# Optimization experiments

Hardware: AMD Instinct MI355X
Metric: run time of the kernel (lower is better)

The kernel has to match this reference:

```python
import jax, jax.numpy as jnp
import numpy as np

# norse LICell parameters: tau_mem_inv given as 1/0.001; others at norse defaults
DT = 0.001          # LICell default dt (module's self.dt is never passed to the cell)
TAU_MEM_INV = 1000.0
TAU_SYN_INV = 200.0
V_LEAK = 0.0


def setup_inputs() -> dict:
    key = jax.random.key(0)
    k1, k2 = jax.random.split(key)
    x = jax.random.normal(k1, (256, 1, 512, 512), dtype=jnp.float32)   # [T, C=1, H, W]
    kernel = jax.random.normal(k2, (5, 5), dtype=jnp.float32)          # square conv kernel
    return {"x": x, "kernel": kernel}


def reference(x, kernel):
    T, C, H, W = x.shape

    # Leaky-integrator (norse li_feed_forward_step) over time:
    #   v' = v + dt*tau_mem_inv*((v_leak - v) + i)
    #   i' = i - dt*tau_syn_inv*i + x_t
    # output at each step is v'.
    def step(carry, xt):
        v, i = carry
        v_new = v + DT * TAU_MEM_INV * ((V_LEAK - v) + i)
        i_new = i - DT * TAU_SYN_INV * i + xt
        return (v_new, i_new), v_new

    zeros = jnp.zeros((C, H, W), x.dtype)
    _, vs = jax.lax.scan(step, (zeros, zeros), x)  # [T, C, H, W]

    # Per-timestep 1->1 channel conv with 'same' padding, batched over T at once.
    k = kernel.shape[0]
    pad = (k - 1) // 2
    w = kernel[None, None]  # [O=1, I=1, k, k]
    out = jax.lax.conv_general_dilated(
        vs, w, window_strides=(1, 1),
        padding=[(pad, pad), (pad, pad)],
        dimension_numbers=("NCHW", "OIHW", "NCHW"),
    )
    return out  # [T, 1, H, W]
```

## Files before the change

### kernel.cpp

```cpp
#include <hip/hip_runtime.h>

#define T_STEPS 256
#define IMG 512
#define HW (IMG * IMG)
#define TW 32
#define TH 8
#define HTW 40
#define HTH 12
#define NCHK 120
#define BUF_DW 512
#define NBUF 12

__device__ __align__(16) float g_zeropage[8] = {0, 0, 0, 0, 0, 0, 0, 0};

typedef const __attribute__((address_space(1))) unsigned int* gptr_t;
typedef __attribute__((address_space(3))) unsigned int* lptr_t;
typedef float vf4 __attribute__((ext_vector_type(4)));

__launch_bounds__(64)
__global__ void conv_li_kernel(const float* __restrict__ x,
                               const float* __restrict__ kern,
                               float* __restrict__ out) {
    __shared__ __align__(16) float lds[NBUF][BUF_DW];
    const int tid = threadIdx.x;
    const int bid = blockIdx.x;
    const int vbid = (bid & 7) * 128 + (bid >> 3);
    const int bx = vbid & 15;
    const int by = vbid >> 4;

    float kw[25];
#pragma unroll
    for (int i = 0; i < 25; ++i)
        kw[i] = __int_as_float(__builtin_amdgcn_readfirstlane(__float_as_int(kern[i])));

    const float* srcA; const float* srcB; bool okA, okB;
    {
        int c = tid;
        int row = c / 10, cc = c - row * 10;
        int gy = by * TH + row - 2, gx = bx * TW + cc * 4 - 4;
        okA = (gy >= 0) && (gy < IMG) && (gx >= 0) && (gx <= IMG - 4);
        srcA = x + (size_t)(okA ? gy : 0) * IMG + (okA ? gx : 0);
        c = tid + 64;
        row = c / 10; cc = c - row * 10;
        gy = by * TH + row - 2; gx = bx * TW + cc * 4 - 4;
        okB = (c < NCHK) && (gy >= 0) && (gy < IMG) && (gx >= 0) && (gx <= IMG - 4);
        srcB = x + (size_t)(okB ? gy : 0) * IMG + (okB ? gx : 0);
    }

    auto GLDS = [&](int bi, int tf) {
        const float* pA = okA ? srcA + (size_t)tf * HW : g_zeropage;
        const float* pB = okB ? srcB + (size_t)tf * HW : g_zeropage;
        __builtin_amdgcn_global_load_lds((gptr_t)pA, (lptr_t)&lds[bi][0], 16, 0, 0);
        __builtin_amdgcn_global_load_lds((gptr_t)pB, (lptr_t)&lds[bi][256], 16, 0, 0);
    };
    auto BATCH = [&](int bufbase, int f0) {
#pragma unroll
        for (int j = 0; j < 4; ++j) {
            int tf = f0 + j; if (tf > T_STEPS - 1) tf = T_STEPS - 1;
            GLDS(bufbase + j, tf);
        }
    };

    const int q = tid & 7;
    const int rr = tid >> 3;
    const size_t obase = (size_t)(by * TH + rr) * IMG + bx * TW + q * 4;

    vf4 st = {0.f, 0.f, 0.f, 0.f};

    auto STEP = [&](int bi, int t) {
        float ax = 0.f, ay = 0.f, az = 0.f, aw = 0.f;
        const float* Bp = &lds[bi][rr * HTW + q * 4];
#pragma unroll
        for (int dy = 0; dy < 5; ++dy) {
            const float* L = Bp + dy * HTW;
            vf4 d0 = *(const vf4*)(L);
            vf4 d1 = *(const vf4*)(L + 4);
            vf4 d2 = *(const vf4*)(L + 8);
            const float e2 = d0.z, e3 = d0.w, e4 = d1.x, e5 = d1.y;
            const float e6 = d1.z, e7 = d1.w, e8 = d2.x, e9 = d2.y;
            const float k0 = kw[dy * 5 + 0], k1 = kw[dy * 5 + 1], k2 = kw[dy * 5 + 2];
            const float k3 = kw[dy * 5 + 3], k4 = kw[dy * 5 + 4];
            ax = fmaf(k0, e2, ax); ax = fmaf(k1, e3, ax); ax = fmaf(k2, e4, ax);
            ax = fmaf(k3, e5, ax); ax = fmaf(k4, e6, ax);
            ay = fmaf(k0, e3, ay); ay = fmaf(k1, e4, ay); ay = fmaf(k2, e5, ay);
            ay = fmaf(k3, e6, ay); ay = fmaf(k4, e7, ay);
            az = fmaf(k0, e4, az); az = fmaf(k1, e5, az); az = fmaf(k2, e6, az);
            az = fmaf(k3, e7, az); az = fmaf(k4, e8, az);
            aw = fmaf(k0, e5, aw); aw = fmaf(k1, e6, aw); aw = fmaf(k2, e7, aw);
            aw = fmaf(k3, e8, aw); aw = fmaf(k4, e9, aw);
        }
        vf4 s = st;
        __builtin_nontemporal_store(s, (vf4*)(out + (size_t)t * HW + obase));
        st.x = st.x - 0.2f * st.x + ax;
        st.y = st.y - 0.2f * st.y + ay;
        st.z = st.z - 0.2f * st.z + az;
        st.w = st.w - 0.2f * st.w + aw;
    };

    BATCH(0, 0);
    BATCH(4, 4);

    asm volatile("s_waitcnt vmcnt(8)" ::: "memory");
    STEP(0, 0); STEP(1, 1); STEP(2, 2); STEP(3, 3);
    BATCH(8, 8);

#pragma clang loop unroll(disable)
    for (int sg = 0; sg < 21; ++sg) {
        const int t0 = 4 + sg * 12;
        asm volatile("s_waitcnt vmcnt(12)" ::: "memory");
        STEP(4, t0 + 0); STEP(5, t0 + 1); STEP(6, t0 + 2); STEP(7, t0 + 3);
        BATCH(0, t0 + 8);
        asm volatile("s_waitcnt vmcnt(12)" ::: "memory");
        STEP(8, t0 + 4); STEP(9, t0 + 5); STEP(10, t0 + 6); STEP(11, t0 + 7);
        BATCH(4, t0 + 12);
        asm volatile("s_waitcnt vmcnt(12)" ::: "memory");
        STEP(0, t0 + 8); STEP(1, t0 + 9); STEP(2, t0 + 10); STEP(3, t0 + 11);
        BATCH(8, t0 + 16);
    }
}

extern "C" void kernel_launch(void* const* d_in, const int* in_sizes, int n_in,
                              void* d_out, int out_size, void* d_ws, size_t ws_size,
                              hipStream_t stream) {
    const float* x = (const float*)d_in[0];
    const float* kern = (const float*)d_in[1];
    float* out = (float*)d_out;

    conv_li_kernel<<<dim3(1024), dim3(64), 0, stream>>>(x, kern, out);
}
```

Before: 98.90 us.

## Widen conv tile to 64 columns with eight outputs per thread and deeper prefetch

Each block now covers a 64x8 output tile instead of 32x8, so the grid is halved and every thread computes eight adjacent outputs. The halo tile is loaded with four direct-to-LDS loads per lane into 12 frames using a padded row stride of 21 chunks. The pipeline now keeps three four-frame batches in flight instead of two. The aim is less redundant halo traffic and more arithmetic per LDS read. The cost is fewer waves per CU, a larger LDS footprint and more registers per thread, which may leave less room to hide memory latency in this bandwidth-bound kernel.

Result: slower. 160.4 us (+62.2%).

```diff
diff --git a/kernel.cpp b/kernel.cpp
--- a/kernel.cpp
+++ b/kernel.cpp
@@ -3,13 +3,13 @@
 #define T_STEPS 256
 #define IMG 512
 #define HW (IMG * IMG)
-#define TW 32
+#define TW 64
 #define TH 8
-#define HTW 40
+#define ROWCHK 18
+#define ROWSTRIDE 21
 #define HTH 12
-#define NCHK 120
-#define BUF_DW 512
-#define NBUF 12
+#define FRAME_DW 1024
+#define NFRAME 12
 
 __device__ __align__(16) float g_zeropage[8] = {0, 0, 0, 0, 0, 0, 0, 0};
 
@@ -21,101 +21,103 @@
 __global__ void conv_li_kernel(const float* __restrict__ x,
                                const float* __restrict__ kern,
                                float* __restrict__ out) {
-    __shared__ __align__(16) float lds[NBUF][BUF_DW];
+    __shared__ __align__(16) float lds[NFRAME * FRAME_DW];
     const int tid = threadIdx.x;
     const int bid = blockIdx.x;
-    const int vbid = (bid & 7) * 128 + (bid >> 3);
-    const int bx = vbid & 15;
-    const int by = vbid >> 4;
+    const int vbid = (bid & 7) * 64 + (bid >> 3);
+    const int bx = vbid & 7;
+    const int by = vbid >> 3;
 
     float kw[25];
 #pragma unroll
     for (int i = 0; i < 25; ++i)
         kw[i] = __int_as_float(__builtin_amdgcn_readfirstlane(__float_as_int(kern[i])));
 
-    const float* srcA; const float* srcB; bool okA, okB;
-    {
-        int c = tid;
-        int row = c / 10, cc = c - row * 10;
-        int gy = by * TH + row - 2, gx = bx * TW + cc * 4 - 4;
-        okA = (gy >= 0) && (gy < IMG) && (gx >= 0) && (gx <= IMG - 4);
-        srcA = x + (size_t)(okA ? gy : 0) * IMG + (okA ? gx : 0);
-        c = tid + 64;
-        row = c / 10; cc = c - row * 10;
-        gy = by * TH + row - 2; gx = bx * TW + cc * 4 - 4;
-        okB = (c < NCHK) && (gy >= 0) && (gy < IMG) && (gx >= 0) && (gx <= IMG - 4);
-        srcB = x + (size_t)(okB ? gy : 0) * IMG + (okB ? gx : 0);
+    const float* src[4]; bool ok[4];
+#pragma unroll
+    for (int k = 0; k < 4; ++k) {
+        int s = k * 64 + tid;
+        int row = s / ROWSTRIDE, cc = s - row * ROWSTRIDE;
+        int gy = by * TH + row - 2;
+        int gx = bx * TW + cc * 4 - 4;
+        ok[k] = (row < HTH) && (cc < ROWCHK) &&
+                (gy >= 0) && (gy < IMG) && (gx >= 0) && (gx <= IMG - 4);
+        src[k] = x + (size_t)(ok[k] ? gy : 0) * IMG + (ok[k] ? gx : 0);
     }
 
-    auto GLDS = [&](int bi, int tf) {
-        const float* pA = okA ? srcA + (size_t)tf * HW : g_zeropage;
-        const float* pB = okB ? srcB + (size_t)tf * HW : g_zeropage;
-        __builtin_amdgcn_global_load_lds((gptr_t)pA, (lptr_t)&lds[bi][0], 16, 0, 0);
-        __builtin_amdgcn_global_load_lds((gptr_t)pB, (lptr_t)&lds[bi][256], 16, 0, 0);
+    auto GLDS = [&](int fi, int tf) {
+        float* fb = &lds[fi * FRAME_DW];
+#pragma unroll
+        for (int k = 0; k < 4; ++k) {
+            const float* p = ok[k] ? src[k] + (size_t)tf * HW : g_zeropage;
+            __builtin_amdgcn_global_load_lds((gptr_t)p, (lptr_t)(fb + k * 256), 16, 0, 0);
+        }
     };
-    auto BATCH = [&](int bufbase, int f0) {
+    auto BATCH = [&](int fbase, int f0) {
 #pragma unroll
         for (int j = 0; j < 4; ++j) {
             int tf = f0 + j; if (tf > T_STEPS - 1) tf = T_STEPS - 1;
-            GLDS(bufbase + j, tf);
+            GLDS(fbase + j, tf);
         }
     };
 
     const int q = tid & 7;
     const int rr = tid >> 3;
-    const size_t obase = (size_t)(by * TH + rr) * IMG + bx * TW + q * 4;
+    const size_t obase = (size_t)(by * TH + rr) * IMG + bx * TW + q * 8;
 
-    vf4 st = {0.f, 0.f, 0.f, 0.f};
+    float st[8] = {0.f, 0.f, 0.f, 0.f, 0.f, 0.f, 0.f, 0.f};
 
-    auto STEP = [&](int bi, int t) {
-        float ax = 0.f, ay = 0.f, az = 0.f, aw = 0.f;
-        const float* Bp = &lds[bi][rr * HTW + q * 4];
+    auto STEP = [&](int fi, int t) {
+        float acc[8] = {0.f, 0.f, 0.f, 0.f, 0.f, 0.f, 0.f, 0.f};
+        const float* F = &lds[fi * FRAME_DW];
 #pragma unroll
         for (int dy = 0; dy < 5; ++dy) {
-            const float* L = Bp + dy * HTW;
-            vf4 d0 = *(const vf4*)(L);
-            vf4 d1 = *(const vf4*)(L + 4);
-            vf4 d2 = *(const vf4*)(L + 8);
-            const float e2 = d0.z, e3 = d0.w, e4 = d1.x, e5 = d1.y;
-            const float e6 = d1.z, e7 = d1.w, e8 = d2.x, e9 = d2.y;
+            const float* L = F + ((rr + dy) * ROWSTRIDE + 2 * q) * 4;
+            vf4 c0 = *(const vf4*)(L);
+            vf4 c1 = *(const vf4*)(L + 4);
+            vf4 c2 = *(const vf4*)(L + 8);
+            vf4 c3 = *(const vf4*)(L + 12);
+            const float w[16] = {c0.x, c0.y, c0.z, c0.w, c1.x, c1.y, c1.z, c1.w,
+                                 c2.x, c2.y, c2.z, c2.w, c3.x, c3.y, c3.z, c3.w};
             const float k0 = kw[dy * 5 + 0], k1 = kw[dy * 5 + 1], k2 = kw[dy * 5 + 2];
             const float k3 = kw[dy * 5 + 3], k4 = kw[dy * 5 + 4];
-            ax = fmaf(k0, e2, ax); ax = fmaf(k1, e3, ax); ax = fmaf(k2, e4, ax);
-            ax = fmaf(k3, e5, ax); ax = fmaf(k4, e6, ax);
-            ay = fmaf(k0, e3, ay); ay = fmaf(k1, e4, ay); ay = fmaf(k2, e5, ay);
-            ay = fmaf(k3, e6, ay); ay = fmaf(k4, e7, ay);
-            az = fmaf(k0, e4, az); az = fmaf(k1, e5, az); az = fmaf(k2, e6, az);
-            az = fmaf(k3, e7, az); az = fmaf(k4, e8, az);
-            aw = fmaf(k0, e5, aw); aw = fmaf(k1, e6, aw); aw = fmaf(k2, e7, aw);
-            aw = fmaf(k3, e8, aw); aw = fmaf(k4, e9, aw);
+#pragma unroll
+            for (int o = 0; o < 8; ++o) {
+                acc[o] = fmaf(k0, w[o + 2], acc[o]);
+                acc[o] = fmaf(k1, w[o + 3], acc[o]);
+                acc[o] = fmaf(k2, w[o + 4], acc[o]);
+                acc[o] = fmaf(k3, w[o + 5], acc[o]);
+                acc[o] = fmaf(k4, w[o + 6], acc[o]);
+            }
         }
-        vf4 s = st;
-        __builtin_nontemporal_store(s, (vf4*)(out + (size_t)t * HW + obase));
-        st.x = st.x - 0.2f * st.x + ax;
-        st.y = st.y - 0.2f * st.y + ay;
-        st.z = st.z - 0.2f * st.z + az;
-        st.w = st.w - 0.2f * st.w + aw;
+        vf4 lo = {st[0], st[1], st[2], st[3]};
+        vf4 hi = {st[4], st[5], st[6], st[7]};
+        float* op = out + (size_t)t * HW + obase;
+        __builtin_nontemporal_store(lo, (vf4*)op);
+        __builtin_nontemporal_store(hi, (vf4*)(op + 4));
+#pragma unroll
+        for (int o = 0; o < 8; ++o)
+            st[o] = st[o] - 0.2f * st[o] + acc[o];
     };
 
     BATCH(0, 0);
     BATCH(4, 4);
-
-    asm volatile("s_waitcnt vmcnt(8)" ::: "memory");
-    STEP(0, 0); STEP(1, 1); STEP(2, 2); STEP(3, 3);
     BATCH(8, 8);
 
+    asm volatile("s_waitcnt vmcnt(32)" ::: "memory");
+    STEP(0, 0); STEP(1, 1); STEP(2, 2); STEP(3, 3);
+    BATCH(0, 12);
+    asm volatile("s_waitcnt vmcnt(40)" ::: "memory");
+    STEP(4, 4); STEP(5, 5); STEP(6, 6); STEP(7, 7);
+    BATCH(4, 16);
 #pragma clang loop unroll(disable)
-    for (int sg = 0; sg < 21; ++sg) {
-        const int t0 = 4 + sg * 12;
-        asm volatile("s_waitcnt vmcnt(12)" ::: "memory");
-        STEP(4, t0 + 0); STEP(5, t0 + 1); STEP(6, t0 + 2); STEP(7, t0 + 3);
-        BATCH(0, t0 + 8);
-        asm volatile("s_waitcnt vmcnt(12)" ::: "memory");
-        STEP(8, t0 + 4); STEP(9, t0 + 5); STEP(10, t0 + 6); STEP(11, t0 + 7);
-        BATCH(4, t0 + 12);
-        asm volatile("s_waitcnt vmcnt(12)" ::: "memory");
-        STEP(0, t0 + 8); STEP(1, t0 + 9); STEP(2, t0 + 10); STEP(3, t0 + 11);
-        BATCH(8, t0 + 16);
+    for (int g = 2; g < 64; ++g) {
+        const int bb = (g % 3) * 4;
+        asm volatile("s_waitcnt vmcnt(48)" ::: "memory");
+        const int t0 = g * 4;
+        STEP(bb + 0, t0 + 0); STEP(bb + 1, t0 + 1);
+        STEP(bb + 2, t0 + 2); STEP(bb + 3, t0 + 3);
+        BATCH(bb, t0 + 12);
     }
 }
 
@@ -126,5 +128,5 @@
     const float* kern = (const float*)d_in[1];
     float* out = (float*)d_out;
 
-    conv_li_kernel<<<dim3(1024), dim3(64), 0, stream>>>(x, kern, out);
+    conv_li_kernel<<<dim3(512), dim3(64), 0, stream>>>(x, kern, out);
 }
```
